# Performance work log

Hardware: AMD Instinct MI355X
Metric: run time of the kernel (lower is better)

The kernel has to match this reference:

```python
import jax, jax.numpy as jnp
import numpy as np

NUM_SAMPLES = 512
FG_FRAC = 0.25
BATCH = 64
N = 131072


def _subsample(key, indicator, labels):
    """Faithful port of BalancedPositiveNegativeSampler._static_subsample.

    indicator: bool [N] sample candidates; labels: bool [N] positive flags.
    Returns int32 [N] indicator of sampled examples (1 = sampled).
    """
    n = indicator.shape[0]
    # Pad indicator with extra False examples so at least NUM_SAMPLES are True.
    num_true = jnp.sum(indicator.astype(jnp.float32))
    additional_false = jnp.cumsum((~indicator).astype(jnp.float32)) <= (NUM_SAMPLES - num_true)
    ind = indicator | additional_false
    # Random shuffle (permutation stored to restore order post-sampling).
    perm = jax.random.permutation(key, n)
    ind_p = ind[perm]
    lab_p = labels[perm]
    # 1-based index where indicator True, 0 otherwise; sign by label.
    idx = jnp.where(ind_p, jnp.arange(1, n + 1, dtype=jnp.int32), jnp.int32(0))
    signed = jnp.where(lab_p, jnp.int32(1), jnp.int32(-1))
    s_idx = idx * signed
    # Descending sort: positives first, then zeros, then negatives (most-negative last).
    sorted_desc = jnp.flip(jnp.sort(s_idx))
    # Balanced pos/neg counts.
    num_pos_avail = jnp.sum((sorted_desc > 0).astype(jnp.int32))
    max_pos = jnp.int32(int(NUM_SAMPLES * FG_FRAC))
    num_pos = jnp.minimum(max_pos, num_pos_avail)
    # Take first num_pos from the start and (NUM_SAMPLES - num_pos) from the end.
    rk = jnp.arange(NUM_SAMPLES, dtype=jnp.int32)
    gather_idx = jnp.where(rk < num_pos, rk, n - NUM_SAMPLES + rk)
    sampled = sorted_desc[gather_idx]
    # Back to 0-based indices; clamp empty slots to 0.
    sampled = jnp.abs(sampled) - 1
    sampled = jnp.where(sampled >= 0, sampled, 0)
    # Indicator in shuffled order, then scatter back through the permutation.
    ind2 = jnp.zeros(n, jnp.int32).at[sampled].set(1)
    out = jnp.zeros(n, jnp.int32).at[perm].set(ind2)
    return out


def setup_inputs() -> dict:
    key = jax.random.key(0)
    k1, k2, k3 = jax.random.split(key, 3)
    positive_matches = jax.random.bernoulli(k1, 0.01, (BATCH, N))
    negative_matches = jax.random.bernoulli(k2, 0.70, (BATCH, N)) & (~positive_matches)
    ignored_matches = jax.random.bernoulli(k3, 0.05, (BATCH, N)) & (~positive_matches) & (~negative_matches)
    return {
        "positive_matches": positive_matches,
        "negative_matches": negative_matches,
        "ignored_matches": ignored_matches,
    }


def reference(positive_matches, negative_matches, ignored_matches):
    b = positive_matches.shape[0]
    candidates = (positive_matches | negative_matches) & (~ignored_matches)
    keys = jax.random.split(jax.random.key(42), b)
    sampled_indicators = jax.vmap(_subsample)(keys, candidates, positive_matches)  # int32 [B, N]
    # Final top_k over {0,1} indicators: selected indices first (ascending), then rest.
    _, selected_indices = jax.lax.top_k(sampled_indicators, NUM_SAMPLES)
    return selected_indices
```

## Files before the change

### kernel.cpp

```cpp
#include <hip/hip_runtime.h>
#include <stdint.h>

#define BATCH 64
#define NN 131072
#define NCOARSE 256
#define SLOT 768
#define CHUNK 4096
#define NSUB 1024
#define EMASK17 0x1FFFFu
#define POSCAP 1024
#define NEGCAP 3072
#define SPOSCAP 96
#define SNEGCAP 224
#define STATICP 128u
#define STATICN 250u

typedef uint32_t u32;
typedef uint64_t u64;

__device__ __forceinline__ u32 rotl32(u32 v, int d) { return (v << d) | (v >> (32 - d)); }

__device__ __forceinline__ void threefry2x32(u32 k0, u32 k1, u32 x0, u32 x1, u32& o0, u32& o1) {
  u32 ks2 = k0 ^ k1 ^ 0x1BD11BDAu;
  x0 += k0; x1 += k1;
#define TF_R(r) { x0 += x1; x1 = rotl32(x1, r); x1 ^= x0; }
  TF_R(13) TF_R(15) TF_R(26) TF_R(6)
  x0 += k1;  x1 += ks2 + 1u;
  TF_R(17) TF_R(29) TF_R(16) TF_R(24)
  x0 += ks2; x1 += k0 + 2u;
  TF_R(13) TF_R(15) TF_R(26) TF_R(6)
  x0 += k0;  x1 += k1 + 3u;
  TF_R(17) TF_R(29) TF_R(16) TF_R(24)
  x0 += k1;  x1 += ks2 + 4u;
  TF_R(13) TF_R(15) TF_R(26) TF_R(6)
  x0 += ks2; x1 += k0 + 5u;
#undef TF_R
  o0 = x0; o1 = x1;
}

__device__ __forceinline__ u32 tf_bits(u32 k0, u32 k1, u32 i) {
  u32 o0, o1;
  threefry2x32(k0, k1, 0u, i, o0, o1);
  return o0 ^ o1;
}

__device__ void batch_round_key(int b, int round, u32& rk0, u32& rk1) {
  u32 kb0, kb1;
  threefry2x32(0u, 42u, 0u, (u32)b, kb0, kb1);
  if (round == 1) { threefry2x32(kb0, kb1, 0u, 1u, rk0, rk1); return; }
  u32 c0, c1;
  threefry2x32(kb0, kb1, 0u, 0u, c0, c1);
  threefry2x32(c0, c1, 0u, 1u, rk0, rk1);
}

__global__ __launch_bounds__(256) void scatterA_kernel(u32* __restrict__ cursor, u64* __restrict__ binned,
                                                       const int* __restrict__ posg, const int* __restrict__ negg,
                                                       const int* __restrict__ igng, int batch0) {
  __shared__ u32 sk[2];
  __shared__ u32 hist[NCOARSE];
  __shared__ u32 lstart[NCOARSE];
  __shared__ u32 gbase[NCOARSE];
  __shared__ u64 staged[CHUNK];
  __shared__ u32 stmp[NCOARSE];
  int g = blockIdx.y;
  int b = batch0 + g;
  int tid = threadIdx.x;
  if (tid == 0) { u32 k0, k1; batch_round_key(b, 1, k0, k1); sk[0] = k0; sk[1] = k1; }
  if (tid < NCOARSE) hist[tid] = 0;
  __syncthreads();
  u32 base = blockIdx.x * CHUNK;
  u64 recs[16]; u32 rr[16];
  const int4* P4 = (const int4*)(posg + (size_t)b * NN);
  const int4* Q4 = (const int4*)(negg + (size_t)b * NN);
  const int4* I4 = (const int4*)(igng + (size_t)b * NN);
#pragma unroll
  for (int j = 0; j < 4; j++) {
    u32 e0 = base + j * 1024 + tid * 4;
    int4 pv = P4[e0 >> 2];
    int4 nv = Q4[e0 >> 2];
    int4 iv = I4[e0 >> 2];
#pragma unroll
    for (int m = 0; m < 4; m++) {
      u32 e = e0 + m;
      int p = (&pv.x)[m] != 0, n = (&nv.x)[m] != 0, ig = (&iv.x)[m] != 0;
      u32 label = ((p | n) && !ig) ? (p ? 1u : 2u) : 0u;
      u32 k1 = tf_bits(sk[0], sk[1], e);
      u32 bin = k1 >> 24;
      rr[j * 4 + m] = atomicAdd(&hist[bin], 1u);
      recs[j * 4 + m] = ((u64)k1 << 19) | ((u64)e << 2) | (u64)label;
    }
  }
  __syncthreads();
  if (tid < NCOARSE) stmp[tid] = hist[tid];
  __syncthreads();
  for (int off = 1; off < NCOARSE; off <<= 1) {
    u32 t = 0;
    if (tid < NCOARSE && tid >= off) t = stmp[tid - off];
    __syncthreads();
    if (tid < NCOARSE) stmp[tid] += t;
    __syncthreads();
  }
  if (tid < NCOARSE) lstart[tid] = stmp[tid] - hist[tid];
  __syncthreads();
#pragma unroll
  for (int j = 0; j < 16; j++) {
    u32 bin = (u32)(recs[j] >> 43);
    staged[lstart[bin] + rr[j]] = recs[j];
  }
  if (tid < NCOARSE) {
    u32 c = hist[tid];
    gbase[tid] = c ? atomicAdd(&cursor[(size_t)g * NCOARSE + tid], c) : 0u;
  }
  __syncthreads();
  u64* bn = binned + (size_t)g * NCOARSE * SLOT;
  for (int s = tid; s < CHUNK; s += 256) {
    u64 v = staged[s];
    u32 bin = (u32)(v >> 43);
    u32 off = gbase[bin] + ((u32)s - lstart[bin]);
    if (off < SLOT) bn[(size_t)bin * SLOT + off] = v;
  }
}

__global__ __launch_bounds__(256) void scanB_kernel(const u32* __restrict__ cursor, u32* __restrict__ starts) {
  __shared__ u32 stmp[NCOARSE];
  __shared__ u32 cnts[NCOARSE];
  int g = blockIdx.x, tid = threadIdx.x;
  u32 v = cursor[(size_t)g * NCOARSE + tid];
  cnts[tid] = v; stmp[tid] = v;
  __syncthreads();
  for (int off = 1; off < NCOARSE; off <<= 1) {
    u32 t = (tid >= off) ? stmp[tid - off] : 0u;
    __syncthreads();
    stmp[tid] += t;
    __syncthreads();
  }
  starts[(size_t)g * NCOARSE + tid] = stmp[tid] - cnts[tid];
}

__global__ __launch_bounds__(512) void passB_kernel(const u32* __restrict__ cursor, const u32* __restrict__ starts,
                                                    const u64* __restrict__ binned,
                                                    u32* __restrict__ posh, u32* __restrict__ negh,
                                                    u32* __restrict__ cnt,
                                                    u64* __restrict__ posbuf, u64* __restrict__ negbuf,
                                                    int batch0) {
  __shared__ u32 sk2[2];
  __shared__ u64 keys[SLOT];
  __shared__ u32 hist[NSUB];
  __shared__ u32 sstart[NSUB];
  __shared__ u32 wtot[8];
  __shared__ u32 lpos[NCOARSE], lneg[NCOARSE];
  __shared__ u64 sposb[SPOSCAP];
  __shared__ u64 snegb[SNEGCAP];
  __shared__ u32 lcb[2], lbase[2];
  int g = blockIdx.y;
  int tid = threadIdx.x;
  if (tid == 0) {
    u32 a, c;
    batch_round_key(batch0 + g, 2, a, c); sk2[0] = a; sk2[1] = c;
    lcb[0] = 0; lcb[1] = 0;
  }
  if (tid < NCOARSE) { lpos[tid] = 0; lneg[tid] = 0; }
  __syncthreads();
  const u64* bn = binned + (size_t)g * NCOARSE * SLOT;
  for (int q = 0; q < 8; q++) {
    u32 bin = blockIdx.x * 8 + q;
    u32 cb = cursor[(size_t)g * NCOARSE + bin];
    if (cb > SLOT) cb = SLOT;
    u32 start = starts[(size_t)g * NCOARSE + bin];
    hist[tid] = 0; hist[tid + 512] = 0;
    __syncthreads();
    u64 mykey[2]; u32 mysr[2];
#pragma unroll
    for (int t = 0; t < 2; t++) {
      int i = tid + t * 512;
      if (i < (int)cb) {
        u64 key = bn[(size_t)bin * SLOT + i];
        u32 sub = (u32)(key >> 33) & 0x3FFu;
        u32 r = atomicAdd(&hist[sub], 1u);
        mykey[t] = key;
        mysr[t] = (sub << 10) | r;
      } else {
        mysr[t] = 0xFFFFFFFFu;
      }
    }
    __syncthreads();
    u32 h0 = hist[2 * tid], h1 = hist[2 * tid + 1];
    u32 s = h0 + h1;
    u32 v = s;
#pragma unroll
    for (int off = 1; off < 64; off <<= 1) {
      u32 t2 = __shfl_up(v, off, 64);
      if ((tid & 63) >= off) v += t2;
    }
    if ((tid & 63) == 63) wtot[tid >> 6] = v;
    __syncthreads();
    u32 woff = 0;
    for (int w = 0; w < (tid >> 6); w++) woff += wtot[w];
    u32 excl = v + woff - s;
    sstart[2 * tid] = excl;
    sstart[2 * tid + 1] = excl + h0;
    __syncthreads();
#pragma unroll
    for (int t = 0; t < 2; t++) {
      if (mysr[t] != 0xFFFFFFFFu)
        keys[sstart[mysr[t] >> 10] + (mysr[t] & 0x3FFu)] = mykey[t];
    }
    __syncthreads();
#pragma unroll
    for (int t = 0; t < 2; t++) {
      int i = tid + t * 512;
      if (i < (int)cb) {
        u64 ki = keys[i];
        u32 sub = (u32)(ki >> 33) & 0x3FFu;
        u32 s0 = sstart[sub], h = hist[sub];
        u32 r = 0;
        for (u32 j = s0; j < s0 + h; j++) {
          if (keys[j] < ki) r++;
        }
        u32 p1 = start + s0 + r;
        u32 label = (u32)ki & 3u;
        if (label) {
          u32 e = (u32)(ki >> 2) & EMASK17;
          u32 k2 = tf_bits(sk2[0], sk2[1], p1);
          u32 b8 = k2 >> 24;
          u64 rec = ((u64)p1 << 32) | e;
          if (label == 1) {
            atomicAdd(&lpos[b8], 1u);
            if (b8 >= STATICP) {
              u32 rr2 = atomicAdd(&lcb[0], 1u);
              if (rr2 < SPOSCAP) sposb[rr2] = rec;
              else {
                u32 s2 = atomicAdd(&cnt[(size_t)g * 16], 1u);
                if (s2 < POSCAP) posbuf[(size_t)g * POSCAP + s2] = rec;
              }
            }
          } else {
            atomicAdd(&lneg[b8], 1u);
            if (b8 >= STATICN) {
              u32 rr2 = atomicAdd(&lcb[1], 1u);
              if (rr2 < SNEGCAP) snegb[rr2] = rec;
              else {
                u32 s2 = atomicAdd(&cnt[(size_t)g * 16 + 1], 1u);
                if (s2 < NEGCAP) negbuf[(size_t)g * NEGCAP + s2] = rec;
              }
            }
          }
        }
      }
    }
    __syncthreads();
  }
  if (tid < NCOARSE) {
    if (lpos[tid]) atomicAdd(&posh[(size_t)g * NCOARSE + tid], lpos[tid]);
  } else if (tid < 2 * NCOARSE) {
    int t = tid - NCOARSE;
    if (lneg[t]) atomicAdd(&negh[(size_t)g * NCOARSE + t], lneg[t]);
  }
  if (tid < 2) {
    u32 n = lcb[tid]; u32 cap = tid ? SNEGCAP : SPOSCAP; if (n > cap) n = cap;
    lbase[tid] = n ? atomicAdd(&cnt[(size_t)g * 16 + tid], n) : 0u;
  }
  __syncthreads();
  {
    u32 n0 = lcb[0]; if (n0 > SPOSCAP) n0 = SPOSCAP;
    for (u32 i = tid; i < n0; i += 512) {
      u32 s2 = lbase[0] + i;
      if (s2 < POSCAP) posbuf[(size_t)g * POSCAP + s2] = sposb[i];
    }
    u32 n1 = lcb[1]; if (n1 > SNEGCAP) n1 = SNEGCAP;
    for (u32 i = tid; i < n1; i += 512) {
      u32 s2 = lbase[1] + i;
      if (s2 < NEGCAP) negbuf[(size_t)g * NEGCAP + s2] = snegb[i];
    }
  }
}

__global__ __launch_bounds__(256) void threshold_kernel(const u32* __restrict__ posh,
                                                        const u32* __restrict__ negh,
                                                        u32* __restrict__ params) {
  int g = blockIdx.x, tid = threadIdx.x;
  __shared__ u32 rp[NCOARSE], rn[NCOARSE];
  rp[tid] = posh[(size_t)g * NCOARSE + tid];
  rn[tid] = negh[(size_t)g * NCOARSE + tid];
  __syncthreads();
  if (tid == 0) {
    u32 np = 0;
    for (int i = 0; i < NCOARSE; i++) np += rp[i];
    u32 qp = np < 128 ? np : 128;
    u32 qn = 512 - qp;
    u32 tp = 256;
    if (qp > 0) {
      u32 cum = 0;
      for (int i = 255; i >= 0; i--) { cum += rp[i]; if (cum >= qp) { tp = (u32)i; break; } }
    }
    u32 tn = 0, cum = 0;
    for (int i = 255; i >= 0; i--) { cum += rn[i]; if (cum >= qn) { tn = (u32)i; break; } }
    u32* pr = params + (size_t)g * 4;
    pr[0] = tp; pr[1] = tn; pr[2] = qp; pr[3] = qn;
  }
}

__global__ __launch_bounds__(1024) void select_final_kernel(const u32* __restrict__ params,
                                                            const u32* __restrict__ cnt,
                                                            const u64* __restrict__ posbuf,
                                                            const u64* __restrict__ negbuf,
                                                            int* __restrict__ out, int batch0) {
  int g = blockIdx.x, tid = threadIdx.x, b = batch0 + g;
  __shared__ u32 sk2[2];
  __shared__ u64 skey[1024];
  __shared__ u32 sval[1024];
  __shared__ int sel[512];
  __shared__ u32 lc;
  if (tid == 0) { u32 a, c; batch_round_key(b, 2, a, c); sk2[0] = a; sk2[1] = c; lc = 0; }
  const u32* pr = params + (size_t)g * 4;
  u32 tp = pr[0], tn = pr[1], qp = pr[2], qn = pr[3];
  u32 cp = cnt[(size_t)g * 16]; if (cp > POSCAP) cp = POSCAP;
  u32 cn = cnt[(size_t)g * 16 + 1]; if (cn > NEGCAP) cn = NEGCAP;
  if (tid < 512) sel[tid] = 0;
  skey[tid] = 0ull; sval[tid] = 0u;
  __syncthreads();

  for (u32 i = tid; i < cp; i += 1024) {
    u64 v = posbuf[(size_t)g * POSCAP + i];
    u32 p1 = (u32)(v >> 32), e = (u32)v;
    u32 k2 = tf_bits(sk2[0], sk2[1], p1);
    if ((k2 >> 24) >= tp) {
      u32 r = atomicAdd(&lc, 1u);
      if (r < 1024) { skey[r] = ((u64)k2 << 32) | p1; sval[r] = e; }
    }
  }
  __syncthreads();
  for (int k = 2; k <= 1024; k <<= 1)
    for (int s = k >> 1; s > 0; s >>= 1) {
      if (tid < 512) {
        int i = ((tid & ~(s - 1)) << 1) | (tid & (s - 1));
        int j = i | s;
        bool up = ((i & k) == 0);
        if ((skey[i] < skey[j]) == up) {
          u64 tk = skey[i]; skey[i] = skey[j]; skey[j] = tk;
          u32 tv = sval[i]; sval[i] = sval[j]; sval[j] = tv;
        }
      }
      __syncthreads();
    }
  if (tid < (int)qp) sel[tid] = (int)sval[tid];
  if (tid == 0) lc = 0;
  __syncthreads();
  skey[tid] = 0ull; sval[tid] = 0u;
  __syncthreads();

  for (u32 i = tid; i < cn; i += 1024) {
    u64 v = negbuf[(size_t)g * NEGCAP + i];
    u32 p1 = (u32)(v >> 32), e = (u32)v;
    u32 k2 = tf_bits(sk2[0], sk2[1], p1);
    if ((k2 >> 24) >= tn) {
      u32 r = atomicAdd(&lc, 1u);
      if (r < 1024) { skey[r] = ((u64)k2 << 32) | p1; sval[r] = e; }
    }
  }
  __syncthreads();
  for (int k = 2; k <= 1024; k <<= 1)
    for (int s = k >> 1; s > 0; s >>= 1) {
      if (tid < 512) {
        int i = ((tid & ~(s - 1)) << 1) | (tid & (s - 1));
        int j = i | s;
        bool up = ((i & k) == 0);
        if ((skey[i] < skey[j]) == up) {
          u64 tk = skey[i]; skey[i] = skey[j]; skey[j] = tk;
          u32 tv = sval[i]; sval[i] = sval[j]; sval[j] = tv;
        }
      }
      __syncthreads();
    }
  if (tid < (int)qn) sel[qp + tid] = (int)sval[tid];
  __syncthreads();

  for (int k = 2; k <= 512; k <<= 1)
    for (int s = k >> 1; s > 0; s >>= 1) {
      if (tid < 256) {
        int i = ((tid & ~(s - 1)) << 1) | (tid & (s - 1));
        int j = i | s;
        bool up = ((i & k) == 0);
        int a = sel[i], c = sel[j];
        if ((a > c) == up) { sel[i] = c; sel[j] = a; }
      }
      __syncthreads();
    }
  if (tid < 512) out[(size_t)b * 512 + tid] = sel[tid];
}

extern "C" void kernel_launch(void* const* d_in, const int* in_sizes, int n_in,
                              void* d_out, int out_size, void* d_ws, size_t ws_size,
                              hipStream_t stream) {
  const int* pos = (const int*)d_in[0];
  const int* neg = (const int*)d_in[1];
  const int* ign = (const int*)d_in[2];
  int* out = (int*)d_out;

  size_t zeroPer = (NCOARSE * 3 + 16) * 4;
  size_t perBatch = zeroPer + (size_t)NCOARSE * SLOT * 8 + NCOARSE * 4 + 16 +
                    (size_t)POSCAP * 8 + (size_t)NEGCAP * 8;
  int G = (int)(ws_size / perBatch);
  if (G > BATCH) G = BATCH;
  if (G < 1) G = 1;

  char* p = (char*)d_ws;
  u32* cursor = (u32*)p;            p += (size_t)G * NCOARSE * 4;
  u32* posh = (u32*)p;              p += (size_t)G * NCOARSE * 4;
  u32* negh = (u32*)p;              p += (size_t)G * NCOARSE * 4;
  u32* cnt = (u32*)p;               p += (size_t)G * 16 * 4;
  size_t zeroBytes = (size_t)p - (size_t)d_ws;
  u64* binned = (u64*)p;            p += (size_t)G * NCOARSE * SLOT * 8;
  u32* starts = (u32*)p;            p += (size_t)G * NCOARSE * 4;
  u32* params = (u32*)p;            p += (size_t)G * 4 * 4;
  u64* posbuf = (u64*)p;            p += (size_t)G * POSCAP * 8;
  u64* negbuf = (u64*)p;            p += (size_t)G * NEGCAP * 8;

  for (int batch0 = 0; batch0 < BATCH; batch0 += G) {
    int Gi = (BATCH - batch0 < G) ? (BATCH - batch0) : G;
    hipMemsetAsync(d_ws, 0, zeroBytes, stream);
    dim3 gridS(NN / CHUNK, Gi);
    scatterA_kernel<<<gridS, 256, 0, stream>>>(cursor, binned, pos, neg, ign, batch0);
    scanB_kernel<<<Gi, 256, 0, stream>>>(cursor, starts);
    dim3 gridP(NCOARSE / 8, Gi);
    passB_kernel<<<gridP, 512, 0, stream>>>(cursor, starts, binned, posh, negh, cnt, posbuf, negbuf, batch0);
    threshold_kernel<<<Gi, 256, 0, stream>>>(posh, negh, params);
    select_final_kernel<<<Gi, 1024, 0, stream>>>(params, cnt, posbuf, negbuf, out, batch0);
  }
}
```

Baseline: 245.7 us.

## Fuse threshold into select kernel and replace bitonic sorts with rank sorts

Removes the separate threshold kernel and computes the histogram thresholds inside the select kernel using a wavefront-shuffle suffix scan and atomicMax. It also replaces the three bitonic sorts, each with many barrier-separated stages, with O(n) per-thread rank counting in shared memory. The aim is to cut one launch per batch group and most of the __syncthreads steps. In exchange each thread does O(n) shared-memory reads, and the packing of wave totals into 16 bits assumes per-wave counts below 65536.

```diff
diff --git a/kernel.cpp b/kernel.cpp
--- a/kernel.cpp
+++ b/kernel.cpp
@@ -275,78 +275,84 @@
   }
 }
 
-__global__ __launch_bounds__(256) void threshold_kernel(const u32* __restrict__ posh,
-                                                        const u32* __restrict__ negh,
-                                                        u32* __restrict__ params) {
-  int g = blockIdx.x, tid = threadIdx.x;
-  __shared__ u32 rp[NCOARSE], rn[NCOARSE];
-  rp[tid] = posh[(size_t)g * NCOARSE + tid];
-  rn[tid] = negh[(size_t)g * NCOARSE + tid];
-  __syncthreads();
-  if (tid == 0) {
-    u32 np = 0;
-    for (int i = 0; i < NCOARSE; i++) np += rp[i];
-    u32 qp = np < 128 ? np : 128;
-    u32 qn = 512 - qp;
-    u32 tp = 256;
-    if (qp > 0) {
-      u32 cum = 0;
-      for (int i = 255; i >= 0; i--) { cum += rp[i]; if (cum >= qp) { tp = (u32)i; break; } }
-    }
-    u32 tn = 0, cum = 0;
-    for (int i = 255; i >= 0; i--) { cum += rn[i]; if (cum >= qn) { tn = (u32)i; break; } }
-    u32* pr = params + (size_t)g * 4;
-    pr[0] = tp; pr[1] = tn; pr[2] = qp; pr[3] = qn;
-  }
-}
-
-__global__ __launch_bounds__(1024) void select_final_kernel(const u32* __restrict__ params,
+__global__ __launch_bounds__(1024) void select_final_kernel(const u32* __restrict__ posh,
+                                                            const u32* __restrict__ negh,
                                                             const u32* __restrict__ cnt,
                                                             const u64* __restrict__ posbuf,
                                                             const u64* __restrict__ negbuf,
                                                             int* __restrict__ out, int batch0) {
   int g = blockIdx.x, tid = threadIdx.x, b = batch0 + g;
   __shared__ u32 sk2[2];
-  __shared__ u64 skey[1024];
-  __shared__ u32 sval[1024];
+  __shared__ u64 key[1024];
+  __shared__ u32 val[1024];
   __shared__ int sel[512];
-  __shared__ u32 lc;
-  if (tid == 0) { u32 a, c; batch_round_key(b, 2, a, c); sk2[0] = a; sk2[1] = c; lc = 0; }
-  const u32* pr = params + (size_t)g * 4;
-  u32 tp = pr[0], tn = pr[1], qp = pr[2], qn = pr[3];
+  __shared__ u32 wtot[4];
+  __shared__ u32 sh_np, sh_tp, sh_tn, sh_nc;
+  if (tid == 0) {
+    u32 a, c; batch_round_key(b, 2, a, c); sk2[0] = a; sk2[1] = c;
+    sh_tp = 0; sh_tn = 0; sh_nc = 0;
+  }
+  __syncthreads();
+
+  u32 myspos = 0, mysneg = 0;
+  if (tid < NCOARSE) {
+    u32 vp = posh[(size_t)g * NCOARSE + (NCOARSE - 1 - tid)];
+    u32 vn = negh[(size_t)g * NCOARSE + (NCOARSE - 1 - tid)];
+    u32 sp2 = vp, sn2 = vn;
+#pragma unroll
+    for (int off = 1; off < 64; off <<= 1) {
+      u32 tp2 = __shfl_up(sp2, off, 64);
+      u32 tn2 = __shfl_up(sn2, off, 64);
+      if ((tid & 63) >= off) { sp2 += tp2; sn2 += tn2; }
+    }
+    if ((tid & 63) == 63) wtot[tid >> 6] = (sp2 & 0xFFFFu) | (sn2 << 16);
+    myspos = sp2; mysneg = sn2;
+  }
+  __syncthreads();
+  if (tid < NCOARSE) {
+    for (int w = 0; w < (tid >> 6); w++) {
+      u32 t2 = wtot[w];
+      myspos += t2 & 0xFFFFu;
+      mysneg += t2 >> 16;
+    }
+    if (tid == NCOARSE - 1) sh_np = myspos;
+  }
+  __syncthreads();
+  u32 np = sh_np;
+  u32 qp = np < 128 ? np : 128;
+  u32 qn = 512 - qp;
+  if (tid < NCOARSE) {
+    u32 i = NCOARSE - 1 - tid;
+    if (qp > 0 && myspos >= qp) atomicMax(&sh_tp, i);
+    if (mysneg >= qn) atomicMax(&sh_tn, i);
+  }
+  if (tid < 512) sel[tid] = 0;
+  __syncthreads();
+  u32 tp = sh_tp, tn = sh_tn;
   u32 cp = cnt[(size_t)g * 16]; if (cp > POSCAP) cp = POSCAP;
   u32 cn = cnt[(size_t)g * 16 + 1]; if (cn > NEGCAP) cn = NEGCAP;
-  if (tid < 512) sel[tid] = 0;
-  skey[tid] = 0ull; sval[tid] = 0u;
-  __syncthreads();
 
   for (u32 i = tid; i < cp; i += 1024) {
     u64 v = posbuf[(size_t)g * POSCAP + i];
     u32 p1 = (u32)(v >> 32), e = (u32)v;
     u32 k2 = tf_bits(sk2[0], sk2[1], p1);
-    if ((k2 >> 24) >= tp) {
-      u32 r = atomicAdd(&lc, 1u);
-      if (r < 1024) { skey[r] = ((u64)k2 << 32) | p1; sval[r] = e; }
-    }
-  }
-  __syncthreads();
-  for (int k = 2; k <= 1024; k <<= 1)
-    for (int s = k >> 1; s > 0; s >>= 1) {
-      if (tid < 512) {
-        int i = ((tid & ~(s - 1)) << 1) | (tid & (s - 1));
-        int j = i | s;
-        bool up = ((i & k) == 0);
-        if ((skey[i] < skey[j]) == up) {
-          u64 tk = skey[i]; skey[i] = skey[j]; skey[j] = tk;
-          u32 tv = sval[i]; sval[i] = sval[j]; sval[j] = tv;
-        }
-      }
-      __syncthreads();
-    }
-  if (tid < (int)qp) sel[tid] = (int)sval[tid];
-  if (tid == 0) lc = 0;
-  __syncthreads();
-  skey[tid] = 0ull; sval[tid] = 0u;
+    if (qp > 0 && (k2 >> 24) >= tp) {
+      u32 r = atomicAdd(&sh_nc, 1u);
+      if (r < 1024) { key[r] = ((u64)k2 << 32) | p1; val[r] = e; }
+    }
+  }
+  __syncthreads();
+  {
+    u32 nc = sh_nc; if (nc > 1024) nc = 1024;
+    if (tid < (int)nc) {
+      u64 mk = key[tid];
+      u32 rank = 0;
+      for (u32 j = 0; j < nc; j++) rank += (key[j] > mk);
+      if (rank < qp) sel[rank] = (int)val[tid];
+    }
+  }
+  __syncthreads();
+  if (tid == 0) sh_nc = 0;
   __syncthreads();
 
   for (u32 i = tid; i < cn; i += 1024) {
@@ -354,39 +360,28 @@
     u32 p1 = (u32)(v >> 32), e = (u32)v;
     u32 k2 = tf_bits(sk2[0], sk2[1], p1);
     if ((k2 >> 24) >= tn) {
-      u32 r = atomicAdd(&lc, 1u);
-      if (r < 1024) { skey[r] = ((u64)k2 << 32) | p1; sval[r] = e; }
-    }
-  }
-  __syncthreads();
-  for (int k = 2; k <= 1024; k <<= 1)
-    for (int s = k >> 1; s > 0; s >>= 1) {
-      if (tid < 512) {
-        int i = ((tid & ~(s - 1)) << 1) | (tid & (s - 1));
-        int j = i | s;
-        bool up = ((i & k) == 0);
-        if ((skey[i] < skey[j]) == up) {
-          u64 tk = skey[i]; skey[i] = skey[j]; skey[j] = tk;
-          u32 tv = sval[i]; sval[i] = sval[j]; sval[j] = tv;
-        }
-      }
-      __syncthreads();
-    }
-  if (tid < (int)qn) sel[qp + tid] = (int)sval[tid];
-  __syncthreads();
-
-  for (int k = 2; k <= 512; k <<= 1)
-    for (int s = k >> 1; s > 0; s >>= 1) {
-      if (tid < 256) {
-        int i = ((tid & ~(s - 1)) << 1) | (tid & (s - 1));
-        int j = i | s;
-        bool up = ((i & k) == 0);
-        int a = sel[i], c = sel[j];
-        if ((a > c) == up) { sel[i] = c; sel[j] = a; }
-      }
-      __syncthreads();
-    }
-  if (tid < 512) out[(size_t)b * 512 + tid] = sel[tid];
+      u32 r = atomicAdd(&sh_nc, 1u);
+      if (r < 1024) { key[r] = ((u64)k2 << 32) | p1; val[r] = e; }
+    }
+  }
+  __syncthreads();
+  {
+    u32 nc = sh_nc; if (nc > 1024) nc = 1024;
+    if (tid < (int)nc) {
+      u64 mk = key[tid];
+      u32 rank = 0;
+      for (u32 j = 0; j < nc; j++) rank += (key[j] > mk);
+      if (rank < qn) sel[qp + rank] = (int)val[tid];
+    }
+  }
+  __syncthreads();
+
+  if (tid < 512) {
+    int v = sel[tid];
+    u32 rank = 0;
+    for (int j = 0; j < 512; j++) rank += (sel[j] < v);
+    out[(size_t)b * 512 + rank] = v;
+  }
 }
 
 extern "C" void kernel_launch(void* const* d_in, const int* in_sizes, int n_in,
@@ -398,7 +393,7 @@
   int* out = (int*)d_out;
 
   size_t zeroPer = (NCOARSE * 3 + 16) * 4;
-  size_t perBatch = zeroPer + (size_t)NCOARSE * SLOT * 8 + NCOARSE * 4 + 16 +
+  size_t perBatch = zeroPer + (size_t)NCOARSE * SLOT * 8 + NCOARSE * 4 +
                     (size_t)POSCAP * 8 + (size_t)NEGCAP * 8;
   int G = (int)(ws_size / perBatch);
   if (G > BATCH) G = BATCH;
@@ -412,7 +407,6 @@
   size_t zeroBytes = (size_t)p - (size_t)d_ws;
   u64* binned = (u64*)p;            p += (size_t)G * NCOARSE * SLOT * 8;
   u32* starts = (u32*)p;            p += (size_t)G * NCOARSE * 4;
-  u32* params = (u32*)p;            p += (size_t)G * 4 * 4;
   u64* posbuf = (u64*)p;            p += (size_t)G * POSCAP * 8;
   u64* negbuf = (u64*)p;            p += (size_t)G * NEGCAP * 8;
 
@@ -424,7 +418,6 @@
     scanB_kernel<<<Gi, 256, 0, stream>>>(cursor, starts);
     dim3 gridP(NCOARSE / 8, Gi);
     passB_kernel<<<gridP, 512, 0, stream>>>(cursor, starts, binned, posh, negh, cnt, posbuf, negbuf, batch0);
-    threshold_kernel<<<Gi, 256, 0, stream>>>(posh, negh, params);
-    select_final_kernel<<<Gi, 1024, 0, stream>>>(params, cnt, posbuf, negbuf, out, batch0);
-  }
-}
+    select_final_kernel<<<Gi, 1024, 0, stream>>>(posh, negh, cnt, posbuf, negbuf, out, batch0);
+  }
+}
```

After: 240.6 us. -2.1%, faster.
